# Performance work log

Measured on AMD Instinct MI355X. Metric: run time of the kernel, lower is better.

## Reference

```python
import jax, jax.numpy as jnp
import numpy as np

EPS = 1e-10

def _feature_map(x):
    # fm(None) defaults to elu(x) + 1 (canonical linear-attention feature map)
    return jax.nn.elu(x) + 1.0

def setup_inputs() -> dict:
    key = jax.random.key(0)
    k1, k2, k3 = jax.random.split(key, 3)
    N, L, H, D = 4, 8192, 16, 64
    return {
        "queries": jax.random.normal(k1, (N, L, H, D), dtype=jnp.float32),
        "keys": jax.random.normal(k2, (N, L, H, D), dtype=jnp.float32),
        "values": jax.random.normal(k3, (N, L, H, D), dtype=jnp.float32),
    }

def reference(queries, keys, values):
    Q = _feature_map(queries)  # [n,l,h,d]
    K = _feature_map(keys)     # [n,s,h,d]
    # KV reduction over sequence: [n,h,m,d]
    KV = jnp.einsum('nshd,nshm->nhmd', K, values)
    # Normalizer: 1 / (Q . sum_s K) + eps (eps added AFTER reciprocal, as in source)
    Z = 1.0 / jnp.einsum('nlhd,nhd->nlh', Q, K.sum(axis=1)) + EPS
    # Output: [n,l,h,m]
    out = jnp.einsum('nlhd,nhmd,nlh->nlhm', Q, KV, Z)
    return out
```

## Files before the change

kernel.cpp:

```cpp
#include <hip/hip_runtime.h>


#define EPSV      1e-10f
#define L_SEQ     8192
#define NH_TOT    64
#define ROWSTRIDE 1024
#define KV_STRIDE 4160
#define SLICE     (NH_TOT * KV_STRIDE)
#define CH_SPLIT  32
#define QSTRIDE   68
#define WSTRIDE   68

__device__ __forceinline__ float fm(float x) {
    return x > 0.0f ? x + 1.0f : __expf(x);
}

__global__ __launch_bounds__(256, 2) void kv_pass_kernel(
    const float* __restrict__ K, const float* __restrict__ V,
    float* __restrict__ ws, int mode)
{
    const int t     = threadIdx.x;
    const int nh    = blockIdx.x;
    const int chunk = blockIdx.y;
    const int n = nh >> 4, h = nh & 15;
    const int wid  = t >> 6;
    const int lane = t & 63;

    const int row8 = lane >> 3;
    const int oct  = lane & 7;
    const int d0   = row8 << 3;
    const int m0   = oct << 3;

    __shared__ float kws[4][8 * WSTRIDE];
    __shared__ float vws[4][8 * WSTRIDE];
    __shared__ float red[4096];
    __shared__ float ksw[4][64];

    float acc[8][8] = {};
    float ks[8] = {};

    const size_t nbase = (size_t)n * (L_SEQ * ROWSTRIDE) + h * 64;
    const int r0 = chunk * 256 + wid * 64;
    const float* Kst = K + nbase + (size_t)(r0 + row8) * ROWSTRIDE + oct * 8;
    const float* Vst = V + nbase + (size_t)(r0 + row8) * ROWSTRIDE + oct * 8;

    const int wofs = oct * WSTRIDE + row8 * 8;
    const int krd  = row8 * WSTRIDE;
    const int vrd  = oct * WSTRIDE;

    float4 kr0 = *reinterpret_cast<const float4*>(Kst);
    float4 kr1 = *reinterpret_cast<const float4*>(Kst + 4);
    float4 vr0 = *reinterpret_cast<const float4*>(Vst);
    float4 vr1 = *reinterpret_cast<const float4*>(Vst + 4);

#pragma unroll 1
    for (int tile = 0; tile < 8; ++tile) {
        float4 kf0, kf1;
        kf0.x = fm(kr0.x); kf0.y = fm(kr0.y); kf0.z = fm(kr0.z); kf0.w = fm(kr0.w);
        kf1.x = fm(kr1.x); kf1.y = fm(kr1.y); kf1.z = fm(kr1.z); kf1.w = fm(kr1.w);
        ks[0] += kf0.x; ks[1] += kf0.y; ks[2] += kf0.z; ks[3] += kf0.w;
        ks[4] += kf1.x; ks[5] += kf1.y; ks[6] += kf1.z; ks[7] += kf1.w;
        *reinterpret_cast<float4*>(&kws[wid][wofs])     = kf0;
        *reinterpret_cast<float4*>(&kws[wid][wofs + 4]) = kf1;
        *reinterpret_cast<float4*>(&vws[wid][wofs])     = vr0;
        *reinterpret_cast<float4*>(&vws[wid][wofs + 4]) = vr1;

        if (tile < 7) {
            const float* kp = Kst + (size_t)(tile + 1) * (8 * ROWSTRIDE);
            const float* vp = Vst + (size_t)(tile + 1) * (8 * ROWSTRIDE);
            kr0 = *reinterpret_cast<const float4*>(kp);
            kr1 = *reinterpret_cast<const float4*>(kp + 4);
            vr0 = *reinterpret_cast<const float4*>(vp);
            vr1 = *reinterpret_cast<const float4*>(vp + 4);
        }

#pragma unroll
        for (int r = 0; r < 8; ++r) {
            const float4 ka = *reinterpret_cast<const float4*>(&kws[wid][krd + r * 8]);
            const float4 kb = *reinterpret_cast<const float4*>(&kws[wid][krd + r * 8 + 4]);
            const float4 va = *reinterpret_cast<const float4*>(&vws[wid][vrd + r * 8]);
            const float4 vb = *reinterpret_cast<const float4*>(&vws[wid][vrd + r * 8 + 4]);
#define ACC8(AI, KC)                                                     \
            acc[AI][0] += (KC) * va.x; acc[AI][1] += (KC) * va.y;        \
            acc[AI][2] += (KC) * va.z; acc[AI][3] += (KC) * va.w;        \
            acc[AI][4] += (KC) * vb.x; acc[AI][5] += (KC) * vb.y;        \
            acc[AI][6] += (KC) * vb.z; acc[AI][7] += (KC) * vb.w;
            ACC8(0, ka.x) ACC8(1, ka.y) ACC8(2, ka.z) ACC8(3, ka.w)
            ACC8(4, kb.x) ACC8(5, kb.y) ACC8(6, kb.z) ACC8(7, kb.w)
#undef ACC8
        }
    }

#pragma unroll
    for (int j = 0; j < 8; ++j) {
        ks[j] += __shfl_xor(ks[j], 8);
        ks[j] += __shfl_xor(ks[j], 16);
        ks[j] += __shfl_xor(ks[j], 32);
    }
    if (lane < 8) {
#pragma unroll
        for (int j = 0; j < 8; ++j) ksw[wid][lane * 8 + j] = ks[j];
    }

    for (int w = 0; w < 4; ++w) {
        if (wid == w) {
#pragma unroll
            for (int i = 0; i < 8; ++i) {
                float* p = &red[(d0 + i) * 64 + m0];
                float4 a0 = make_float4(acc[i][0], acc[i][1], acc[i][2], acc[i][3]);
                float4 a1 = make_float4(acc[i][4], acc[i][5], acc[i][6], acc[i][7]);
                if (w != 0) {
                    const float4 b0 = *reinterpret_cast<const float4*>(p);
                    const float4 b1 = *reinterpret_cast<const float4*>(p + 4);
                    a0.x += b0.x; a0.y += b0.y; a0.z += b0.z; a0.w += b0.w;
                    a1.x += b1.x; a1.y += b1.y; a1.z += b1.z; a1.w += b1.w;
                }
                *reinterpret_cast<float4*>(p)     = a0;
                *reinterpret_cast<float4*>(p + 4) = a1;
            }
        }
        __syncthreads();
    }

    float* dst = ws + (size_t)(mode ? (chunk * NH_TOT + nh) : nh) * KV_STRIDE;
    if (mode) {
#pragma unroll
        for (int i = 0; i < 4; ++i)
            *reinterpret_cast<float4*>(dst + t * 16 + i * 4) =
                *reinterpret_cast<const float4*>(&red[t * 16 + i * 4]);
        if (t < 64)
            dst[4096 + t] = ksw[0][t] + ksw[1][t] + ksw[2][t] + ksw[3][t];
    } else {
#pragma unroll
        for (int i = 0; i < 16; ++i)
            atomicAdd(dst + t * 16 + i, red[t * 16 + i]);
        if (t < 64)
            atomicAdd(dst + 4096 + t, ksw[0][t] + ksw[1][t] + ksw[2][t] + ksw[3][t]);
    }
}

__global__ __launch_bounds__(256) void reduce_kernel(float* __restrict__ ws, int CH)
{
    const int idx = blockIdx.x * 256 + threadIdx.x;
    float s = 0.f;
    for (int c = 0; c < CH; ++c) s += ws[(size_t)c * SLICE + idx];
    ws[idx] = s;
}

__global__ __launch_bounds__(256) void out_kernel(
    const float* __restrict__ Q, const float* __restrict__ KVg,
    float* __restrict__ out)
{
    const int t      = threadIdx.x;
    const int lchunk = blockIdx.x;
    const int nh     = blockIdx.y;
    const int n = nh >> 4, h = nh & 15;

    __shared__ float Ql[64 * QSTRIDE];
    __shared__ float KVl[4096];
    __shared__ float Ks[64];
    __shared__ float zl[64];

    const float* kvrow = KVg + (size_t)nh * KV_STRIDE;

#pragma unroll
    for (int j = 0; j < 4; ++j) {
        reinterpret_cast<float4*>(KVl)[t + 256 * j] =
            reinterpret_cast<const float4*>(kvrow)[t + 256 * j];
    }
    if (t < 16) {
        reinterpret_cast<float4*>(Ks)[t] =
            reinterpret_cast<const float4*>(kvrow + 4096)[t];
    }
    __syncthreads();

    const int lane16 = t & 15, grp = t >> 4;
    const int dq = lane16 << 2;
    const float4 ks4 = *reinterpret_cast<const float4*>(&Ks[dq]);
    const size_t qbase = ((size_t)n * L_SEQ + lchunk * 64) * ROWSTRIDE + h * 64;
#pragma unroll
    for (int p = 0; p < 4; ++p) {
        const int rr = p * 16 + grp;
        const float4 qg = *reinterpret_cast<const float4*>(Q + qbase + (size_t)rr * ROWSTRIDE + dq);
        float4 qf;
        qf.x = fm(qg.x); qf.y = fm(qg.y); qf.z = fm(qg.z); qf.w = fm(qg.w);
        *reinterpret_cast<float4*>(&Ql[rr * QSTRIDE + dq]) = qf;
        float dp = qf.x * ks4.x + qf.y * ks4.y + qf.z * ks4.z + qf.w * ks4.w;
        dp += __shfl_xor(dp, 1);
        dp += __shfl_xor(dp, 2);
        dp += __shfl_xor(dp, 4);
        dp += __shfl_xor(dp, 8);
        if (lane16 == 0) zl[rr] = 1.0f / dp + EPSV;
    }
    __syncthreads();

    const int r0 = grp << 2;
    const int c0 = lane16 << 2;
    float acc[4][4] = {};
#pragma unroll 2
    for (int d = 0; d < 64; d += 4) {
        const float4 b0 = *reinterpret_cast<const float4*>(&KVl[(d + 0) * 64 + c0]);
        const float4 b1 = *reinterpret_cast<const float4*>(&KVl[(d + 1) * 64 + c0]);
        const float4 b2 = *reinterpret_cast<const float4*>(&KVl[(d + 2) * 64 + c0]);
        const float4 b3 = *reinterpret_cast<const float4*>(&KVl[(d + 3) * 64 + c0]);
#define DO_ROW(i) do {                                                              \
        const float4 q = *reinterpret_cast<const float4*>(&Ql[(r0 + (i)) * QSTRIDE + d]); \
        acc[i][0] += q.x * b0.x + q.y * b1.x + q.z * b2.x + q.w * b3.x;             \
        acc[i][1] += q.x * b0.y + q.y * b1.y + q.z * b2.y + q.w * b3.y;             \
        acc[i][2] += q.x * b0.z + q.y * b1.z + q.z * b2.z + q.w * b3.z;             \
        acc[i][3] += q.x * b0.w + q.y * b1.w + q.z * b2.w + q.w * b3.w;             \
    } while (0)
        DO_ROW(0); DO_ROW(1); DO_ROW(2); DO_ROW(3);
#undef DO_ROW
    }

#pragma unroll
    for (int i = 0; i < 4; ++i) {
        const float z = zl[r0 + i];
        float4 o;
        o.x = acc[i][0] * z; o.y = acc[i][1] * z; o.z = acc[i][2] * z; o.w = acc[i][3] * z;
        *reinterpret_cast<float4*>(out + qbase + (size_t)(r0 + i) * ROWSTRIDE + c0) = o;
    }
}

extern "C" void kernel_launch(void* const* d_in, const int* in_sizes, int n_in,
                              void* d_out, int out_size, void* d_ws, size_t ws_size,
                              hipStream_t stream) {
    const float* Q = (const float*)d_in[0];
    const float* K = (const float*)d_in[1];
    const float* V = (const float*)d_in[2];
    float* out = (float*)d_out;
    float* ws  = (float*)d_ws;

    const size_t per_slice = (size_t)SLICE * sizeof(float);
    const bool split = ws_size >= per_slice * CH_SPLIT;

    if (split) {
        kv_pass_kernel<<<dim3(NH_TOT, CH_SPLIT), 256, 0, stream>>>(K, V, ws, 1);
        reduce_kernel<<<SLICE / 256, 256, 0, stream>>>(ws, CH_SPLIT);
    } else {
        hipMemsetAsync(ws, 0, per_slice, stream);
        kv_pass_kernel<<<dim3(NH_TOT, CH_SPLIT), 256, 0, stream>>>(K, V, ws, 0);
    }
    out_kernel<<<dim3(L_SEQ / 64, NH_TOT), 256, 0, stream>>>(Q, ws, out);
}
```

Measured before the change: 191.5 us.

## Shrink KV-pass LDS staging to 4-row tiles and alias it with reduction buffer

The per-wave staging of K and V now covers 4 rows per tile (16 tiles) instead of 8, with each lane loading a single float4 from K and V instead of two. The staging buffers are aliased onto the reduction buffer, which cuts shared memory per block and may allow more resident blocks. The inner product loop is software-pipelined, with the LDS fragment reads double-buffered ahead of the FMAs. The cost is twice as many loop iterations with less work each, plus an added __syncthreads before the reduction buffer is reused.

After: 195.1 us. No clear change (+1.9%).

```diff
diff --git a/kernel.cpp b/kernel.cpp
--- a/kernel.cpp
+++ b/kernel.cpp
@@ -9,7 +9,9 @@
 #define SLICE     (NH_TOT * KV_STRIDE)
 #define CH_SPLIT  32
 #define QSTRIDE   68
-#define WSTRIDE   68
+#define WSTR      36
+#define WWIN      (8 * WSTR)
+#define WAVEWIN   (2 * WWIN)
 
 __device__ __forceinline__ float fm(float x) {
     return x > 0.0f ? x + 1.0f : __expf(x);
@@ -26,81 +28,95 @@
     const int wid  = t >> 6;
     const int lane = t & 63;
 
-    const int row8 = lane >> 3;
-    const int oct  = lane & 7;
-    const int d0   = row8 << 3;
-    const int m0   = oct << 3;
-
-    __shared__ float kws[4][8 * WSTRIDE];
-    __shared__ float vws[4][8 * WSTRIDE];
-    __shared__ float red[4096];
+    const int d0 = (lane >> 3) << 3;
+    const int m0 = (lane & 7) << 3;
+
+    const int srow = lane >> 4;
+    const int q4   = lane & 15;
+    const int g    = q4 >> 1;
+    const int h2   = q4 & 1;
+
+    __shared__ float smem[4096];
     __shared__ float ksw[4][64];
 
+    float* kws = &smem[wid * WAVEWIN];
+    float* vws = kws + WWIN;
+
     float acc[8][8] = {};
-    float ks[8] = {};
+    float ks[4] = {};
 
     const size_t nbase = (size_t)n * (L_SEQ * ROWSTRIDE) + h * 64;
     const int r0 = chunk * 256 + wid * 64;
-    const float* Kst = K + nbase + (size_t)(r0 + row8) * ROWSTRIDE + oct * 8;
-    const float* Vst = V + nbase + (size_t)(r0 + row8) * ROWSTRIDE + oct * 8;
-
-    const int wofs = oct * WSTRIDE + row8 * 8;
-    const int krd  = row8 * WSTRIDE;
-    const int vrd  = oct * WSTRIDE;
-
-    float4 kr0 = *reinterpret_cast<const float4*>(Kst);
-    float4 kr1 = *reinterpret_cast<const float4*>(Kst + 4);
-    float4 vr0 = *reinterpret_cast<const float4*>(Vst);
-    float4 vr1 = *reinterpret_cast<const float4*>(Vst + 4);
+    const float* Kst = K + nbase + (size_t)(r0 + srow) * ROWSTRIDE + q4 * 4;
+    const float* Vst = V + nbase + (size_t)(r0 + srow) * ROWSTRIDE + q4 * 4;
+
+    const int wofs = g * WSTR + srow * 8 + h2 * 4;
+    const int krd  = (lane >> 3) * WSTR;
+    const int vrd  = (lane & 7) * WSTR;
+
+    float4 kr = *reinterpret_cast<const float4*>(Kst);
+    float4 vr = *reinterpret_cast<const float4*>(Vst);
+
+#define RD_FRAG(KA, KB, VA, VB, R)                                          \
+    KA = *reinterpret_cast<const float4*>(&kws[krd + (R) * 8]);             \
+    KB = *reinterpret_cast<const float4*>(&kws[krd + (R) * 8 + 4]);         \
+    VA = *reinterpret_cast<const float4*>(&vws[vrd + (R) * 8]);             \
+    VB = *reinterpret_cast<const float4*>(&vws[vrd + (R) * 8 + 4]);
+
+#define ACC8(AI, KC, VA, VB)                                                \
+    acc[AI][0] += (KC) * (VA).x; acc[AI][1] += (KC) * (VA).y;               \
+    acc[AI][2] += (KC) * (VA).z; acc[AI][3] += (KC) * (VA).w;               \
+    acc[AI][4] += (KC) * (VB).x; acc[AI][5] += (KC) * (VB).y;               \
+    acc[AI][6] += (KC) * (VB).z; acc[AI][7] += (KC) * (VB).w;
+
+#define FMA_FRAG(KA, KB, VA, VB)                                            \
+    ACC8(0, (KA).x, VA, VB) ACC8(1, (KA).y, VA, VB)                         \
+    ACC8(2, (KA).z, VA, VB) ACC8(3, (KA).w, VA, VB)                         \
+    ACC8(4, (KB).x, VA, VB) ACC8(5, (KB).y, VA, VB)                         \
+    ACC8(6, (KB).z, VA, VB) ACC8(7, (KB).w, VA, VB)
 
 #pragma unroll 1
-    for (int tile = 0; tile < 8; ++tile) {
-        float4 kf0, kf1;
-        kf0.x = fm(kr0.x); kf0.y = fm(kr0.y); kf0.z = fm(kr0.z); kf0.w = fm(kr0.w);
-        kf1.x = fm(kr1.x); kf1.y = fm(kr1.y); kf1.z = fm(kr1.z); kf1.w = fm(kr1.w);
-        ks[0] += kf0.x; ks[1] += kf0.y; ks[2] += kf0.z; ks[3] += kf0.w;
-        ks[4] += kf1.x; ks[5] += kf1.y; ks[6] += kf1.z; ks[7] += kf1.w;
-        *reinterpret_cast<float4*>(&kws[wid][wofs])     = kf0;
-        *reinterpret_cast<float4*>(&kws[wid][wofs + 4]) = kf1;
-        *reinterpret_cast<float4*>(&vws[wid][wofs])     = vr0;
-        *reinterpret_cast<float4*>(&vws[wid][wofs + 4]) = vr1;
-
-        if (tile < 7) {
-            const float* kp = Kst + (size_t)(tile + 1) * (8 * ROWSTRIDE);
-            const float* vp = Vst + (size_t)(tile + 1) * (8 * ROWSTRIDE);
-            kr0 = *reinterpret_cast<const float4*>(kp);
-            kr1 = *reinterpret_cast<const float4*>(kp + 4);
-            vr0 = *reinterpret_cast<const float4*>(vp);
-            vr1 = *reinterpret_cast<const float4*>(vp + 4);
+    for (int tile = 0; tile < 16; ++tile) {
+        float4 kf;
+        kf.x = fm(kr.x); kf.y = fm(kr.y); kf.z = fm(kr.z); kf.w = fm(kr.w);
+        ks[0] += kf.x; ks[1] += kf.y; ks[2] += kf.z; ks[3] += kf.w;
+        *reinterpret_cast<float4*>(&kws[wofs]) = kf;
+        *reinterpret_cast<float4*>(&vws[wofs]) = vr;
+
+        if (tile < 15) {
+            const float* kp = Kst + (size_t)(tile + 1) * (4 * ROWSTRIDE);
+            const float* vp = Vst + (size_t)(tile + 1) * (4 * ROWSTRIDE);
+            kr = *reinterpret_cast<const float4*>(kp);
+            vr = *reinterpret_cast<const float4*>(vp);
         }
 
-#pragma unroll
-        for (int r = 0; r < 8; ++r) {
-            const float4 ka = *reinterpret_cast<const float4*>(&kws[wid][krd + r * 8]);
-            const float4 kb = *reinterpret_cast<const float4*>(&kws[wid][krd + r * 8 + 4]);
-            const float4 va = *reinterpret_cast<const float4*>(&vws[wid][vrd + r * 8]);
-            const float4 vb = *reinterpret_cast<const float4*>(&vws[wid][vrd + r * 8 + 4]);
-#define ACC8(AI, KC)                                                     \
-            acc[AI][0] += (KC) * va.x; acc[AI][1] += (KC) * va.y;        \
-            acc[AI][2] += (KC) * va.z; acc[AI][3] += (KC) * va.w;        \
-            acc[AI][4] += (KC) * vb.x; acc[AI][5] += (KC) * vb.y;        \
-            acc[AI][6] += (KC) * vb.z; acc[AI][7] += (KC) * vb.w;
-            ACC8(0, ka.x) ACC8(1, ka.y) ACC8(2, ka.z) ACC8(3, ka.w)
-            ACC8(4, kb.x) ACC8(5, kb.y) ACC8(6, kb.z) ACC8(7, kb.w)
+        float4 kaA, kbA, vaA, vbA, kaB, kbB, vaB, vbB;
+        RD_FRAG(kaA, kbA, vaA, vbA, 0)
+        RD_FRAG(kaB, kbB, vaB, vbB, 1)
+        FMA_FRAG(kaA, kbA, vaA, vbA)
+        RD_FRAG(kaA, kbA, vaA, vbA, 2)
+        FMA_FRAG(kaB, kbB, vaB, vbB)
+        RD_FRAG(kaB, kbB, vaB, vbB, 3)
+        FMA_FRAG(kaA, kbA, vaA, vbA)
+        FMA_FRAG(kaB, kbB, vaB, vbB)
+    }
+
+#undef RD_FRAG
 #undef ACC8
-        }
-    }
-
-#pragma unroll
-    for (int j = 0; j < 8; ++j) {
-        ks[j] += __shfl_xor(ks[j], 8);
+#undef FMA_FRAG
+
+#pragma unroll
+    for (int j = 0; j < 4; ++j) {
         ks[j] += __shfl_xor(ks[j], 16);
         ks[j] += __shfl_xor(ks[j], 32);
     }
-    if (lane < 8) {
-#pragma unroll
-        for (int j = 0; j < 8; ++j) ksw[wid][lane * 8 + j] = ks[j];
-    }
+    if (lane < 16) {
+        *reinterpret_cast<float4*>(&ksw[wid][lane * 4]) =
+            make_float4(ks[0], ks[1], ks[2], ks[3]);
+    }
+
+    __syncthreads();
+    float* red = smem;
 
     for (int w = 0; w < 4; ++w) {
         if (wid == w) {
```
